# Performance work log

Measured on AMD Instinct MI355X. Metric: run time of the kernel, lower is better.

The kernel has to match this reference:

```python
import jax, jax.numpy as jnp
import numpy as np

FACTOR = 5  # routing softmax power


def setup_inputs() -> dict:
    key = jax.random.key(0)
    kq, kk, kv = jax.random.split(key, 3)
    B, L, S, H, E, D = 2, 2048, 2048, 16, 64, 64
    queries = jax.random.normal(kq, (B, L, H, E), dtype=jnp.float32)
    keys = jax.random.normal(kk, (B, S, H, E), dtype=jnp.float32)
    values = jax.random.normal(kv, (B, S, H, D), dtype=jnp.float32)
    return {"queries": queries, "keys": keys, "values": values}


def reference(queries, keys, values):
    # NOTE: original computes scale = 1/sqrt(E) but never applies it; faithful.
    # Original computes the same unscaled QK^T twice; compute once and reuse.
    scores = jnp.einsum('blhe,bshe->bhls', queries, keys)  # [B,H,L,S]
    dense = jax.nn.softmax(scores, axis=-1)
    routing = dense ** FACTOR  # softmax(scores)**factor == routing_scores
    combined = (routing + dense) * 0.5
    sparse = combined / jnp.sum(combined, axis=-1, keepdims=True)
    V = jnp.einsum('bhls,bshd->blhd', sparse, values)  # [B,L,H,D]
    return V
```

## Files before the change

### kernel.cpp

```cpp
#include <hip/hip_runtime.h>
#include <math.h>


typedef _Float16 h8 __attribute__((ext_vector_type(8)));
typedef float f4 __attribute__((ext_vector_type(4)));
typedef float f16v __attribute__((ext_vector_type(16)));
typedef unsigned int u4v __attribute__((ext_vector_type(4)));

constexpr int Sc = 2048, Hc = 16;
constexpr int KB = 64, NT = Sc / KB;
constexpr float LOG2E = 1.4426950408889634f;

__device__ __forceinline__ f16v mm32(h8 a, h8 b, f16v c) {
  return __builtin_amdgcn_mfma_f32_32x32x16_f16(a, b, c, 0, 0, 0);
}
__device__ __forceinline__ unsigned pku(float a, float b) {
  return __builtin_bit_cast(unsigned, __builtin_amdgcn_cvt_pkrtz(a, b));
}

__global__ __launch_bounds__(256, 2) void dsa_mfma(
    const float* __restrict__ Q, const float* __restrict__ K,
    const float* __restrict__ V, float* __restrict__ O) {
  __shared__ __align__(16) _Float16 Ks[2][64 * 64];
  __shared__ __align__(16) _Float16 Vts[2][64 * 64];

  const int tid = threadIdx.x;
  const int w = tid >> 6, lane = tid & 63, lm = lane & 31, hi = lane >> 5;
  const int swz = (lm & 7) << 3;

  const int blk = blockIdx.x;
  const int ww = (blk & 7) * 64 + (blk >> 3);
  const int qtb = ww & 15, bh = ww >> 4;
  const int b = bh >> 4, h = bh & 15;

  const size_t base = ((size_t)b * Sc * Hc + h) * 64;
  const float* Qb = Q + base;
  const float* Kb = K + base;
  const float* Vb = V + base;
  const int q0 = qtb * 128 + w * 32;

  h8 qf[4];
#pragma unroll
  for (int s = 0; s < 4; ++s) {
    const float* p = Qb + (size_t)(q0 + lm) * 1024 + s * 16 + hi * 8;
    f4 a = *(const f4*)p, c = *(const f4*)(p + 4);
#pragma unroll
    for (int i = 0; i < 4; ++i) {
      qf[s][i] = (_Float16)(a[i] * LOG2E);
      qf[s][4 + i] = (_Float16)(c[i] * LOG2E);
    }
  }
  h8 ones;
#pragma unroll
  for (int i = 0; i < 8; ++i) ones[i] = (_Float16)1.0f;

  f16v O1[2] = {}, O5[2] = {};
  f16v S1a = {}, S5a = {};
  float mr = -INFINITY;

  f4 kf[4];
  float vreg[2][8];
  const int krow = tid & 63, kq = tid >> 6;
  const int vd = tid & 63, vo0 = (tid >> 6) * 2;

  auto LOADK = [&](int k0) {
#pragma unroll
    for (int j = 0; j < 4; ++j)
      kf[j] = *(const f4*)(Kb + (size_t)(k0 + krow) * 1024 + kq * 16 + 4 * j);
  };
  auto LOADV = [&](int k0) {
#pragma unroll
    for (int i = 0; i < 2; ++i) {
      const float* p = Vb + (size_t)(k0 + (vo0 + i) * 8) * 1024 + vd;
#pragma unroll
      for (int j = 0; j < 8; ++j) vreg[i][j] = p[(size_t)j * 1024];
    }
  };
  auto STORE = [&](int buf) {
#pragma unroll
    for (int i = 0; i < 2; ++i) {
      u4v wv = {pku(kf[2 * i][0], kf[2 * i][1]), pku(kf[2 * i][2], kf[2 * i][3]),
                pku(kf[2 * i + 1][0], kf[2 * i + 1][1]), pku(kf[2 * i + 1][2], kf[2 * i + 1][3])};
      int col = (kq * 16 + 8 * i) ^ ((krow & 7) << 3);
      *(h8*)&Ks[buf][krow * 64 + col] = __builtin_bit_cast(h8, wv);
    }
#pragma unroll
    for (int i = 0; i < 2; ++i) {
      u4v wv = {pku(vreg[i][0], vreg[i][1]), pku(vreg[i][2], vreg[i][3]),
                pku(vreg[i][4], vreg[i][5]), pku(vreg[i][6], vreg[i][7])};
      int col = ((vo0 + i) * 8) ^ ((vd & 7) << 3);
      *(h8*)&Vts[buf][vd * 64 + col] = __builtin_bit_cast(h8, wv);
    }
  };

  LOADK(0);
  LOADV(0);
  STORE(0);
  LOADK(KB);
  LOADV(KB);
  __syncthreads();

#pragma unroll 1
  for (int t = 0; t < NT; ++t) {
    const int cur = t & 1;
    if (t + 1 < NT) STORE(cur ^ 1);
    if (t + 2 < NT) {
      LOADK((t + 2) * KB);
      LOADV((t + 2) * KB);
    }

    f16v sc[2] = {};
    __builtin_amdgcn_s_setprio(1);
#pragma unroll
    for (int s = 0; s < 4; ++s) {
      h8 a0 = *(const h8*)&Ks[cur][lm * 64 + ((s * 16 + hi * 8) ^ swz)];
      h8 a1 = *(const h8*)&Ks[cur][(32 + lm) * 64 + ((s * 16 + hi * 8) ^ swz)];
      sc[0] = mm32(a0, qf[s], sc[0]);
      sc[1] = mm32(a1, qf[s], sc[1]);
    }
    __builtin_amdgcn_s_setprio(0);

    float m16[16];
#pragma unroll
    for (int r = 0; r < 16; ++r) m16[r] = fmaxf(sc[0][r], sc[1][r]);
#pragma unroll
    for (int d = 8; d >= 1; d >>= 1)
#pragma unroll
      for (int r = 0; r < d; ++r) m16[r] = fmaxf(m16[r], m16[r + d]);
    float tm = fmaxf(m16[0], __shfl_xor(m16[0], 32));
    if (__any(tm > mr)) {
      float nm = fmaxf(mr, tm);
      float f = __builtin_amdgcn_exp2f(mr - nm);
      float f2 = f * f, f5 = f2 * f2 * f;
      mr = nm;
      S1a *= f;
      S5a *= f5;
#pragma unroll
      for (int dt = 0; dt < 2; ++dt) {
        O1[dt] *= f;
        O5[dt] *= f5;
      }
    }

#pragma unroll
    for (int s = 0; s < 4; ++s) {
      const int kh = s >> 1, s8 = (s & 1) * 8;
      float e[8];
#pragma unroll
      for (int j = 0; j < 8; ++j) e[j] = __builtin_amdgcn_exp2f(sc[kh][s8 + j] - mr);
      auto rA = __builtin_amdgcn_permlane32_swap(pku(e[0], e[1]), pku(e[4], e[5]), false, false);
      auto rB = __builtin_amdgcn_permlane32_swap(pku(e[2], e[3]), pku(e[6], e[7]), false, false);
      u4v bwE = {(unsigned)rA[0], (unsigned)rB[0], (unsigned)rA[1], (unsigned)rB[1]};
      h8 bE = __builtin_bit_cast(h8, bwE);
      h8 b2 = bE * bE, b4 = b2 * b2, b5 = b4 * bE;

      h8 v0 = *(const h8*)&Vts[cur][lm * 64 + ((s * 16 + hi * 8) ^ swz)];
      h8 v1 = *(const h8*)&Vts[cur][(32 + lm) * 64 + ((s * 16 + hi * 8) ^ swz)];
      __builtin_amdgcn_s_setprio(1);
      O1[0] = mm32(v0, bE, O1[0]);
      O1[1] = mm32(v1, bE, O1[1]);
      S1a = mm32(ones, bE, S1a);
      O5[0] = mm32(v0, b5, O5[0]);
      O5[1] = mm32(v1, b5, O5[1]);
      S5a = mm32(ones, b5, S5a);
      __builtin_amdgcn_s_setprio(0);
    }

    __syncthreads();
  }

  const float z = S1a[0], z2 = z * z, z4 = z2 * z2;
  const float inv = 1.0f / (S5a[0] + z4 * S1a[0]);
#pragma unroll
  for (int dt = 0; dt < 2; ++dt)
#pragma unroll
    for (int i = 0; i < 4; ++i) {
      f4 o;
#pragma unroll
      for (int j = 0; j < 4; ++j)
        o[j] = (O5[dt][4 * i + j] + z4 * O1[dt][4 * i + j]) * inv;
      *(f4*)(O + base + (size_t)(q0 + lm) * 1024 + dt * 32 + 8 * i + 4 * hi) = o;
    }
}

extern "C" void kernel_launch(void* const* d_in, const int* in_sizes, int n_in,
                              void* d_out, int out_size, void* d_ws, size_t ws_size,
                              hipStream_t stream) {
  const float* q = (const float*)d_in[0];
  const float* k = (const float*)d_in[1];
  const float* v = (const float*)d_in[2];
  float* o = (float*)d_out;
  dsa_mfma<<<dim3(512), dim3(256), 0, stream>>>(q, k, v, o);
}
```

Baseline: 91.35 us.

## Process two key tiles per iteration with a four-deep LDS ring buffer

The main loop now handles two 64-key tiles per iteration. The K/V shared-memory staging grows from two buffers to a four-slot ring, and QK scores for both tiles are computed before a single running-max update and rescale. Global loads and LDS stores for later tiles are interleaved between the two PV phases, and there is now one barrier per two tiles. This aims to cut barrier, max-reduction and rescale overhead and to hide more load latency. The cost is doubled LDS use per block and more live score registers, which could limit occupancy or cause spills.

```diff
diff --git a/kernel.cpp b/kernel.cpp
--- a/kernel.cpp
+++ b/kernel.cpp
@@ -21,8 +21,7 @@
 __global__ __launch_bounds__(256, 2) void dsa_mfma(
     const float* __restrict__ Q, const float* __restrict__ K,
     const float* __restrict__ V, float* __restrict__ O) {
-  __shared__ __align__(16) _Float16 Ks[2][64 * 64];
-  __shared__ __align__(16) _Float16 Vts[2][64 * 64];
+  __shared__ __align__(16) _Float16 smem[4][2][64 * 64];
 
   const int tid = threadIdx.x;
   const int w = tid >> 6, lane = tid & 63, lm = lane & 31, hi = lane >> 5;
@@ -77,19 +76,63 @@
     }
   };
   auto STORE = [&](int buf) {
+    _Float16* Ks = &smem[buf][0][0];
+    _Float16* Vts = &smem[buf][1][0];
 #pragma unroll
     for (int i = 0; i < 2; ++i) {
       u4v wv = {pku(kf[2 * i][0], kf[2 * i][1]), pku(kf[2 * i][2], kf[2 * i][3]),
                 pku(kf[2 * i + 1][0], kf[2 * i + 1][1]), pku(kf[2 * i + 1][2], kf[2 * i + 1][3])};
       int col = (kq * 16 + 8 * i) ^ ((krow & 7) << 3);
-      *(h8*)&Ks[buf][krow * 64 + col] = __builtin_bit_cast(h8, wv);
+      *(h8*)&Ks[krow * 64 + col] = __builtin_bit_cast(h8, wv);
     }
 #pragma unroll
     for (int i = 0; i < 2; ++i) {
       u4v wv = {pku(vreg[i][0], vreg[i][1]), pku(vreg[i][2], vreg[i][3]),
                 pku(vreg[i][4], vreg[i][5]), pku(vreg[i][6], vreg[i][7])};
       int col = ((vo0 + i) * 8) ^ ((vd & 7) << 3);
-      *(h8*)&Vts[buf][vd * 64 + col] = __builtin_bit_cast(h8, wv);
+      *(h8*)&Vts[vd * 64 + col] = __builtin_bit_cast(h8, wv);
+    }
+  };
+
+  auto QK = [&](int cur, f16v sc[2]) {
+    const _Float16* Ks = &smem[cur][0][0];
+    sc[0] = f16v{};
+    sc[1] = f16v{};
+    __builtin_amdgcn_s_setprio(1);
+#pragma unroll
+    for (int s = 0; s < 4; ++s) {
+      h8 a0 = *(const h8*)&Ks[lm * 64 + ((s * 16 + hi * 8) ^ swz)];
+      h8 a1 = *(const h8*)&Ks[(32 + lm) * 64 + ((s * 16 + hi * 8) ^ swz)];
+      sc[0] = mm32(a0, qf[s], sc[0]);
+      sc[1] = mm32(a1, qf[s], sc[1]);
+    }
+    __builtin_amdgcn_s_setprio(0);
+  };
+
+  auto PVX = [&](int cur, f16v sc[2]) {
+    const _Float16* Vts = &smem[cur][1][0];
+#pragma unroll
+    for (int s = 0; s < 4; ++s) {
+      const int kh = s >> 1, s8 = (s & 1) * 8;
+      float e[8];
+#pragma unroll
+      for (int j = 0; j < 8; ++j) e[j] = __builtin_amdgcn_exp2f(sc[kh][s8 + j] - mr);
+      auto rA = __builtin_amdgcn_permlane32_swap(pku(e[0], e[1]), pku(e[4], e[5]), false, false);
+      auto rB = __builtin_amdgcn_permlane32_swap(pku(e[2], e[3]), pku(e[6], e[7]), false, false);
+      u4v bwE = {(unsigned)rA[0], (unsigned)rB[0], (unsigned)rA[1], (unsigned)rB[1]};
+      h8 bE = __builtin_bit_cast(h8, bwE);
+      h8 b2 = bE * bE, b4 = b2 * b2, b5 = b4 * bE;
+
+      h8 v0 = *(const h8*)&Vts[lm * 64 + ((s * 16 + hi * 8) ^ swz)];
+      h8 v1 = *(const h8*)&Vts[(32 + lm) * 64 + ((s * 16 + hi * 8) ^ swz)];
+      __builtin_amdgcn_s_setprio(1);
+      O1[0] = mm32(v0, bE, O1[0]);
+      O1[1] = mm32(v1, bE, O1[1]);
+      S1a = mm32(ones, bE, S1a);
+      O5[0] = mm32(v0, b5, O5[0]);
+      O5[1] = mm32(v1, b5, O5[1]);
+      S5a = mm32(ones, b5, S5a);
+      __builtin_amdgcn_s_setprio(0);
     }
   };
 
@@ -98,31 +141,27 @@
   STORE(0);
   LOADK(KB);
   LOADV(KB);
+  STORE(1);
+  LOADK(2 * KB);
+  LOADV(2 * KB);
   __syncthreads();
 
 #pragma unroll 1
-  for (int t = 0; t < NT; ++t) {
-    const int cur = t & 1;
-    if (t + 1 < NT) STORE(cur ^ 1);
-    if (t + 2 < NT) {
-      LOADK((t + 2) * KB);
-      LOADV((t + 2) * KB);
-    }
-
-    f16v sc[2] = {};
-    __builtin_amdgcn_s_setprio(1);
-#pragma unroll
-    for (int s = 0; s < 4; ++s) {
-      h8 a0 = *(const h8*)&Ks[cur][lm * 64 + ((s * 16 + hi * 8) ^ swz)];
-      h8 a1 = *(const h8*)&Ks[cur][(32 + lm) * 64 + ((s * 16 + hi * 8) ^ swz)];
-      sc[0] = mm32(a0, qf[s], sc[0]);
-      sc[1] = mm32(a1, qf[s], sc[1]);
-    }
-    __builtin_amdgcn_s_setprio(0);
+  for (int t = 0; t < NT; t += 2) {
+    if (t + 2 < NT) STORE((t + 2) & 3);
+    if (t + 3 < NT) {
+      LOADK((t + 3) * KB);
+      LOADV((t + 3) * KB);
+    }
+
+    f16v s0[2], s1[2];
+    QK(t & 3, s0);
+    QK((t + 1) & 3, s1);
 
     float m16[16];
 #pragma unroll
-    for (int r = 0; r < 16; ++r) m16[r] = fmaxf(sc[0][r], sc[1][r]);
+    for (int r = 0; r < 16; ++r)
+      m16[r] = fmaxf(fmaxf(s0[0][r], s0[1][r]), fmaxf(s1[0][r], s1[1][r]));
 #pragma unroll
     for (int d = 8; d >= 1; d >>= 1)
 #pragma unroll
@@ -142,29 +181,15 @@
       }
     }
 
-#pragma unroll
-    for (int s = 0; s < 4; ++s) {
-      const int kh = s >> 1, s8 = (s & 1) * 8;
-      float e[8];
-#pragma unroll
-      for (int j = 0; j < 8; ++j) e[j] = __builtin_amdgcn_exp2f(sc[kh][s8 + j] - mr);
-      auto rA = __builtin_amdgcn_permlane32_swap(pku(e[0], e[1]), pku(e[4], e[5]), false, false);
-      auto rB = __builtin_amdgcn_permlane32_swap(pku(e[2], e[3]), pku(e[6], e[7]), false, false);
-      u4v bwE = {(unsigned)rA[0], (unsigned)rB[0], (unsigned)rA[1], (unsigned)rB[1]};
-      h8 bE = __builtin_bit_cast(h8, bwE);
-      h8 b2 = bE * bE, b4 = b2 * b2, b5 = b4 * bE;
-
-      h8 v0 = *(const h8*)&Vts[cur][lm * 64 + ((s * 16 + hi * 8) ^ swz)];
-      h8 v1 = *(const h8*)&Vts[cur][(32 + lm) * 64 + ((s * 16 + hi * 8) ^ swz)];
-      __builtin_amdgcn_s_setprio(1);
-      O1[0] = mm32(v0, bE, O1[0]);
-      O1[1] = mm32(v1, bE, O1[1]);
-      S1a = mm32(ones, bE, S1a);
-      O5[0] = mm32(v0, b5, O5[0]);
-      O5[1] = mm32(v1, b5, O5[1]);
-      S5a = mm32(ones, b5, S5a);
-      __builtin_amdgcn_s_setprio(0);
-    }
+    PVX(t & 3, s0);
+
+    if (t + 3 < NT) STORE((t + 3) & 3);
+    if (t + 4 < NT) {
+      LOADK((t + 4) * KB);
+      LOADV((t + 4) * KB);
+    }
+
+    PVX((t + 1) & 3, s1);
 
     __syncthreads();
   }
```

Result: faster. 86.26 us (-5.6%).
